# Performance work log

Measured on AMD Instinct MI355X. Metric: run time of the kernel, lower is better.

Reference implementation:

```python
import jax, jax.numpy as jnp
import numpy as np

UPDATE_RATE = 0.5
ALIVE_THRESH = 0.1

_SHIFTS = [(di, dj) for di in (-1, 0, 1) for dj in (-1, 0, 1) if not (di == 0 and dj == 0)]

def _laplacian(x):
    # circular 3x3 Laplacian: 8*center - 8 neighbors (wrap-around == circular pad)
    s = x * 8.0
    for di, dj in _SHIFTS:
        s = s - jnp.roll(x, (di, dj), axis=(2, 3))
    return s

def _alive_mask(alpha):
    # max_pool2d(3, stride=1) over circularly padded alpha == max over 3x3 wrap neighborhood
    m = alpha
    for di, dj in _SHIFTS:
        m = jnp.maximum(m, jnp.roll(alpha, (di, dj), axis=(2, 3)))
    return (m > ALIVE_THRESH).astype(alpha.dtype)

def setup_inputs() -> dict:
    key = jax.random.key(0)
    k1, k2, k3, k4, k5 = jax.random.split(key, 5)
    B, CHN, H, W = 4, 16, 512, 512
    PERC_N, HID = 2 * CHN, 192
    x = jax.random.uniform(k1, (B, CHN, H, W), dtype=jnp.float32)
    noise = jax.random.uniform(k2, (B, 1, H, W), dtype=jnp.float32)
    w1_w = jax.random.normal(k3, (HID, PERC_N), dtype=jnp.float32) * 0.1
    w1_b = jax.random.normal(k4, (HID,), dtype=jnp.float32) * 0.1
    w2_w = jax.random.normal(k5, (CHN, HID), dtype=jnp.float32) * 0.1
    return {"x": x, "noise": noise, "w1_w": w1_w, "w1_b": w1_b, "w2_w": w2_w}

def reference(x, noise, w1_w, w1_b, w2_w):
    alive = _alive_mask(x[:, 3:4])                       # [B,1,H,W]
    y = jnp.concatenate([x, _laplacian(x)], axis=1)      # [B,2C,H,W] perception
    h = jax.nn.relu(jnp.einsum('bchw,oc->bohw', y, w1_w) + w1_b[None, :, None, None])
    dx = jnp.einsum('bchw,oc->bohw', h, w2_w)            # [B,C,H,W]
    update_mask = jnp.floor(noise + UPDATE_RATE)         # stochastic per-pixel gate
    return (x + dx * update_mask) * alive
```

## Files before the change

### kernel.cpp

```cpp
#include <hip/hip_runtime.h>


#define HH 512
#define WW 512
#define CC 16
#define HID 192
#define NT 16
#define HW (HH * WW)

typedef _Float16 half8  __attribute__((ext_vector_type(8)));
typedef _Float16 half2v __attribute__((ext_vector_type(2)));
typedef __fp16   fp16x2 __attribute__((ext_vector_type(2)));
typedef float    f32x4  __attribute__((ext_vector_type(4)));
typedef unsigned int u32;

__device__ __forceinline__ u32 h2i(half2v v) { return __builtin_bit_cast(u32, v); }
__device__ __forceinline__ half2v i2h(u32 v) { return __builtin_bit_cast(half2v, v); }
__device__ __forceinline__ u32 pkrtz(float a, float b) {
    return __builtin_bit_cast(u32, __builtin_amdgcn_cvt_pkrtz(a, b));
}
__device__ __forceinline__ u32 fi(float f) { return __builtin_bit_cast(u32, f); }
__device__ __forceinline__ float if_(u32 v) { return __builtin_bit_cast(float, v); }

#define SWZ_P15 0x1F0
#define SWZ_P0  0x0010
#define SWZ_LO  0x000F

#define SWZ(v, patt) ((u32)__builtin_amdgcn_ds_swizzle((int)(v), (patt)))
#define DPP_UP1(old, src) ((u32)__builtin_amdgcn_update_dpp((int)(old), (int)(src), 0x111, 0xF, 0xF, false))
#define DPP_DN1(old, src) ((u32)__builtin_amdgcn_update_dpp((int)(old), (int)(src), 0x101, 0xF, 0xF, false))

__global__ __launch_bounds__(256, 2) void nca_mfma_kernel(
    const float* __restrict__ x,
    const float* __restrict__ noise,
    const float* __restrict__ w1w,
    const float* __restrict__ w1b,
    const float* __restrict__ w2w,
    float* __restrict__ out)
{
    __shared__ __align__(16) float bl[HID];
    const int tid  = threadIdx.x;
    const int lane = tid & 63;
    const int wid  = tid >> 6;
    const int p    = lane & 15;
    const int gq   = lane >> 4;

    const int bid = blockIdx.x;
    const int lin = (bid & 7) * 128 + (bid >> 3);
    const int gr    = __builtin_amdgcn_readfirstlane(lin * 4 + wid);
    const int b     = gr >> 10;
    const int rem   = gr & 1023;
    const int i     = rem >> 1;
    const int start = (rem & 1) * (WW / 2);

    for (int k = tid; k < HID; k += 256) bl[k] = w1b[k];
    __syncthreads();

    half8 w1f[12];
    #pragma unroll
    for (int t = 0; t < 12; ++t) {
        const float* src = w1w + (16 * t + p) * 32 + 8 * gq;
        #pragma unroll
        for (int e = 0; e < 8; ++e) w1f[t][e] = (_Float16)src[e];
    }
    const int pi_p = (p & 3) | ((p & 4) << 1) | ((p & 8) >> 1);
    half8 w2f[6];
    #pragma unroll
    for (int f = 0; f < 6; ++f) {
        const float* s0 = w2w + pi_p * HID + 32 * f + 4 * gq;
        #pragma unroll
        for (int e = 0; e < 4; ++e) {
            w2f[f][e]     = (_Float16)s0[e];
            w2f[f][4 + e] = (_Float16)s0[16 + e];
        }
    }

    const int im = (i == 0) ? HH - 1 : i - 1;
    const int ip = (i == HH - 1) ? 0 : i + 1;
    const int rT = im * WW, rM = i * WW, rB = ip * WW;
    const float* xbch = x + ((size_t)b * CC + 8 * (gq & 1)) * HW;
    const float* pT = xbch + rT;
    const float* pM = xbch + rM;
    const float* pB = xbch + rB;
    const float* nrow = noise + (size_t)b * HW + rM;
    float* orow = out + (size_t)b * CC * HW + rM;

    const bool hiSel = (gq >= 2);
    const int gqsw = ((gq & 1) << 1) | (gq >> 1);

    auto loadRaw = [&](int col, float r[24]) {
        #pragma unroll
        for (int e = 0; e < 8; ++e) {
            r[3 * e + 0] = pT[e * HW + col];
            r[3 * e + 1] = pM[e * HW + col];
            r[3 * e + 2] = pB[e * HW + col];
        }
    };
    auto combine = [&](const float r[24], half2v pcs[4], half2v pm[4],
                       float mx[4], float& cm) {
        #pragma unroll
        for (int w = 0; w < 4; ++w) {
            const float cs0 = r[6 * w + 0] + r[6 * w + 1] + r[6 * w + 2];
            const float cs1 = r[6 * w + 3] + r[6 * w + 4] + r[6 * w + 5];
            pcs[w] = i2h(pkrtz(cs0, cs1));
            pm[w]  = i2h(pkrtz(r[6 * w + 1], r[6 * w + 4]));
        }
        #pragma unroll
        for (int j = 0; j < 4; ++j)
            mx[j] = hiSel ? r[3 * (j + 4) + 1] : r[3 * j + 1];
        cm = fmaxf(fmaxf(r[9], r[10]), r[11]);
    };

    half2v pcsA[4], pcsB[4], pcsC[4], pmB[4], pmC[4];
    float  mxB[4], mxC[4];
    float  cmA, cmB, cmC;
    float  nzB, nzC;
    float  rr[24];

    {
        float rh[24]; half2v dum[4]; float dmx[4];
        loadRaw((start - 1) & (WW - 1), rh);
        combine(rh, pcsA, dum, dmx, cmA);
        float r0[24];
        loadRaw(start + p, r0);
        combine(r0, pcsB, pmB, mxB, cmB);
        float r1[24];
        loadRaw(start + 16 + p, r1);
        combine(r1, pcsC, pmC, mxC, cmC);
        nzB = nrow[start + p];
        nzC = nrow[start + 16 + p];
    }

    const f32x4* blv = (const f32x4*)bl;
    const half2v k9 = {(_Float16)9.0f, (_Float16)9.0f};
    const bool isCenter = (gq < 2);
    const u32 PZ = 0;

    #pragma unroll 4
    for (int t = 0; t < NT; ++t) {
        const int colP = (start + 16 * (t + 2) + p) & (WW - 1);
        loadRaw(colP, rr);
        const float nzD = nrow[colP];

        union { half8 v; u32 iw[4]; } yf;
        #pragma unroll
        for (int w = 0; w < 4; ++w) {
            const u32 bw = h2i(pcsB[w]);
            const u32 pl = SWZ(h2i(pcsA[w]), SWZ_P15);
            const u32 pr = SWZ(h2i(pcsC[w]), SWZ_P0);
            const u32 lft = DPP_UP1(pl, bw);
            const u32 rgt = DPP_DN1(pr, bw);
            const half2v s9  = i2h(lft) + i2h(bw) + i2h(rgt);
            const half2v lap = k9 * pmB[w] - s9;
            yf.iw[w] = isCenter ? h2i(pmB[w]) : h2i(lap);
        }

        const u32 pml = SWZ(fi(cmA), SWZ_P15);
        const u32 pmr = SWZ(fi(cmC), SWZ_P0);
        const float ml = if_(DPP_UP1(pml, fi(cmB)));
        const float mr = if_(DPP_DN1(pmr, fi(cmB)));
        const float rmax  = fmaxf(fmaxf(ml, cmB), mr);
        const float av    = if_(SWZ(fi(rmax), SWZ_LO));
        const float alive = (av > 0.1f) ? 1.0f : 0.0f;
        const float um    = floorf(nzB + 0.5f);

        f32x4 acc2a = {0.f, 0.f, 0.f, 0.f}, acc2b = {0.f, 0.f, 0.f, 0.f};
        #pragma unroll
        for (int f = 0; f < 6; ++f) {
            const f32x4 ba = blv[8 * f + gq];
            const f32x4 bb = blv[8 * f + 4 + gq];
            const f32x4 a1 = __builtin_amdgcn_mfma_f32_16x16x32_f16(w1f[2 * f],     yf.v, ba, 0, 0, 0);
            const f32x4 a2 = __builtin_amdgcn_mfma_f32_16x16x32_f16(w1f[2 * f + 1], yf.v, bb, 0, 0, 0);
            union { half8 v; u32 iw[4]; } hf;
            #pragma unroll
            for (int w = 0; w < 4; ++w) {
                const f32x4& aa = (w < 2) ? a1 : a2;
                const u32 pk = pkrtz(aa[2 * (w & 1)], aa[2 * (w & 1) + 1]);
                u32 rl;
                asm("v_pk_max_f16 %0, %1, %2" : "=v"(rl) : "v"(pk), "v"(PZ));
                hf.iw[w] = rl;
            }
            if (f & 1) acc2b = __builtin_amdgcn_mfma_f32_16x16x32_f16(w2f[f], hf.v, acc2b, 0, 0, 0);
            else       acc2a = __builtin_amdgcn_mfma_f32_16x16x32_f16(w2f[f], hf.v, acc2a, 0, 0, 0);
        }

        const int col = start + 16 * t + p;
        #pragma unroll
        for (int r = 0; r < 4; ++r) {
            const float dx = acc2a[r] + acc2b[r];
            orow[(size_t)(4 * gqsw + r) * HW + col] = (mxB[r] + dx * um) * alive;
        }

        half2v pcsD[4], pmD[4]; float mxD[4]; float cmD;
        combine(rr, pcsD, pmD, mxD, cmD);
        #pragma unroll
        for (int w = 0; w < 4; ++w) {
            pcsA[w] = pcsB[w];
            pcsB[w] = pcsC[w]; pmB[w] = pmC[w];
            pcsC[w] = pcsD[w]; pmC[w] = pmD[w];
        }
        #pragma unroll
        for (int j = 0; j < 4; ++j) { mxB[j] = mxC[j]; mxC[j] = mxD[j]; }
        cmA = cmB; cmB = cmC; cmC = cmD;
        nzB = nzC; nzC = nzD;
    }
}

extern "C" void kernel_launch(void* const* d_in, const int* in_sizes, int n_in,
                              void* d_out, int out_size, void* d_ws, size_t ws_size,
                              hipStream_t stream)
{
    const float* x     = (const float*)d_in[0];
    const float* noise = (const float*)d_in[1];
    const float* w1w   = (const float*)d_in[2];
    const float* w1b   = (const float*)d_in[3];
    const float* w2w   = (const float*)d_in[4];
    float* out = (float*)d_out;

    nca_mfma_kernel<<<1024, 256, 0, stream>>>(x, noise, w1w, w1b, w2w, out);
}
```

Measured before the change: 59.07 us.

## Fold Laplacian center term into W1, prefetch deeper, reuse fp16 center values

The 9*center part of the Laplacian is folded into the first-layer weights at load time, so the loop feeds the raw 3x3 neighbour sum into the MFMA instead of computing 9x−s9 per pixel. Column loads are moved one tile further ahead, so the fetch for column t+3 is in flight while column t is computed. The separate fp32 copy of the residual x is dropped, and the output residual is rebuilt from the packed fp16 center values. This cuts per-pixel ALU work and register pressure, but the residual now carries fp16 round-toward-zero error, and the deeper prefetch keeps more data live in registers.

```diff
diff --git a/kernel.cpp b/kernel.cpp
--- a/kernel.cpp
+++ b/kernel.cpp
@@ -10,7 +10,6 @@
 
 typedef _Float16 half8  __attribute__((ext_vector_type(8)));
 typedef _Float16 half2v __attribute__((ext_vector_type(2)));
-typedef __fp16   fp16x2 __attribute__((ext_vector_type(2)));
 typedef float    f32x4  __attribute__((ext_vector_type(4)));
 typedef unsigned int u32;
 
@@ -56,12 +55,18 @@
     for (int k = tid; k < HID; k += 256) bl[k] = w1b[k];
     __syncthreads();
 
+    const bool isCenter = (gq < 2);
     half8 w1f[12];
     #pragma unroll
     for (int t = 0; t < 12; ++t) {
-        const float* src = w1w + (16 * t + p) * 32 + 8 * gq;
-        #pragma unroll
-        for (int e = 0; e < 8; ++e) w1f[t][e] = (_Float16)src[e];
+        const float* src = w1w + (16 * t + p) * 32;
+        #pragma unroll
+        for (int e = 0; e < 8; ++e) {
+            const int o1 = 8 * gq + e;
+            const int o2 = o1 + (isCenter ? 16 : 0);
+            const float a = src[o1], c = src[o2];
+            w1f[t][e] = (_Float16)(isCenter ? (a + 9.0f * c) : -a);
+        }
     }
     const int pi_p = (p & 3) | ((p & 4) << 1) | ((p & 8) >> 1);
     half8 w2f[6];
@@ -96,8 +101,7 @@
             r[3 * e + 2] = pB[e * HW + col];
         }
     };
-    auto combine = [&](const float r[24], half2v pcs[4], half2v pm[4],
-                       float mx[4], float& cm) {
+    auto combine = [&](const float r[24], half2v pcs[4], half2v pm[4], float& cm) {
         #pragma unroll
         for (int w = 0; w < 4; ++w) {
             const float cs0 = r[6 * w + 0] + r[6 * w + 1] + r[6 * w + 2];
@@ -105,42 +109,41 @@
             pcs[w] = i2h(pkrtz(cs0, cs1));
             pm[w]  = i2h(pkrtz(r[6 * w + 1], r[6 * w + 4]));
         }
-        #pragma unroll
-        for (int j = 0; j < 4; ++j)
-            mx[j] = hiSel ? r[3 * (j + 4) + 1] : r[3 * j + 1];
         cm = fmaxf(fmaxf(r[9], r[10]), r[11]);
     };
 
     half2v pcsA[4], pcsB[4], pcsC[4], pmB[4], pmC[4];
-    float  mxB[4], mxC[4];
     float  cmA, cmB, cmC;
-    float  nzB, nzC;
+    float  nzB, nzC, nzD;
     float  rr[24];
 
     {
-        float rh[24]; half2v dum[4]; float dmx[4];
+        float rh[24]; half2v dum[4];
         loadRaw((start - 1) & (WW - 1), rh);
-        combine(rh, pcsA, dum, dmx, cmA);
+        combine(rh, pcsA, dum, cmA);
         float r0[24];
         loadRaw(start + p, r0);
-        combine(r0, pcsB, pmB, mxB, cmB);
+        combine(r0, pcsB, pmB, cmB);
         float r1[24];
         loadRaw(start + 16 + p, r1);
-        combine(r1, pcsC, pmC, mxC, cmC);
+        combine(r1, pcsC, pmC, cmC);
         nzB = nrow[start + p];
         nzC = nrow[start + 16 + p];
+        loadRaw(start + 32 + p, rr);
+        nzD = nrow[start + 32 + p];
     }
 
     const f32x4* blv = (const f32x4*)bl;
-    const half2v k9 = {(_Float16)9.0f, (_Float16)9.0f};
-    const bool isCenter = (gq < 2);
     const u32 PZ = 0;
 
     #pragma unroll 4
     for (int t = 0; t < NT; ++t) {
-        const int colP = (start + 16 * (t + 2) + p) & (WW - 1);
+        half2v pcsD[4], pmD[4]; float cmD;
+        combine(rr, pcsD, pmD, cmD);
+
+        const int colP = (start + 16 * (t + 3) + p) & (WW - 1);
         loadRaw(colP, rr);
-        const float nzD = nrow[colP];
+        const float nzE = nrow[colP];
 
         union { half8 v; u32 iw[4]; } yf;
         #pragma unroll
@@ -150,9 +153,8 @@
             const u32 pr = SWZ(h2i(pcsC[w]), SWZ_P0);
             const u32 lft = DPP_UP1(pl, bw);
             const u32 rgt = DPP_DN1(pr, bw);
-            const half2v s9  = i2h(lft) + i2h(bw) + i2h(rgt);
-            const half2v lap = k9 * pmB[w] - s9;
-            yf.iw[w] = isCenter ? h2i(pmB[w]) : h2i(lap);
+            const half2v s9 = i2h(lft) + i2h(bw) + i2h(rgt);
+            yf.iw[w] = isCenter ? h2i(pmB[w]) : h2i(s9);
         }
 
         const u32 pml = SWZ(fi(cmA), SWZ_P15);
@@ -184,25 +186,24 @@
             else       acc2a = __builtin_amdgcn_mfma_f32_16x16x32_f16(w2f[f], hf.v, acc2a, 0, 0, 0);
         }
 
+        const half2v xp0 = hiSel ? pmB[2] : pmB[0];
+        const half2v xp1 = hiSel ? pmB[3] : pmB[1];
+        const float xr[4] = {(float)xp0[0], (float)xp0[1], (float)xp1[0], (float)xp1[1]};
         const int col = start + 16 * t + p;
         #pragma unroll
         for (int r = 0; r < 4; ++r) {
             const float dx = acc2a[r] + acc2b[r];
-            orow[(size_t)(4 * gqsw + r) * HW + col] = (mxB[r] + dx * um) * alive;
-        }
-
-        half2v pcsD[4], pmD[4]; float mxD[4]; float cmD;
-        combine(rr, pcsD, pmD, mxD, cmD);
+            orow[(size_t)(4 * gqsw + r) * HW + col] = (xr[r] + dx * um) * alive;
+        }
+
         #pragma unroll
         for (int w = 0; w < 4; ++w) {
             pcsA[w] = pcsB[w];
             pcsB[w] = pcsC[w]; pmB[w] = pmC[w];
             pcsC[w] = pcsD[w]; pmC[w] = pmD[w];
         }
-        #pragma unroll
-        for (int j = 0; j < 4; ++j) { mxB[j] = mxC[j]; mxC[j] = mxD[j]; }
         cmA = cmB; cmB = cmC; cmC = cmD;
-        nzB = nzC; nzC = nzD;
+        nzB = nzC; nzC = nzD; nzD = nzE;
     }
 }
 
```

After: 73.41 us. 24.3% more time.

## Process two adjacent columns per lane with float2 loads and full-row waves

Applied to the files above, without the earlier changes.

Each lane now handles two adjacent pixels using 8-byte vector loads and stores instead of scalar accesses. Each wave processes a full image row, so the grid is halved to 512 blocks and the per-wave halo/prologue overhead is reduced. Horizontal neighbor exchange is restructured so that within-lane pairs avoid cross-lane shuffles and only the outer neighbors use swizzle/DPP. This doubles the MFMA work per iteration and raises register pressure, and the smaller grid (two blocks per CU via launch bounds) may leave parallelism or latency hiding insufficient.

```diff
diff --git a/kernel.cpp b/kernel.cpp
--- a/kernel.cpp
+++ b/kernel.cpp
@@ -10,7 +10,7 @@
 
 typedef _Float16 half8  __attribute__((ext_vector_type(8)));
 typedef _Float16 half2v __attribute__((ext_vector_type(2)));
-typedef __fp16   fp16x2 __attribute__((ext_vector_type(2)));
+typedef float    f32x2  __attribute__((ext_vector_type(2)));
 typedef float    f32x4  __attribute__((ext_vector_type(4)));
 typedef unsigned int u32;
 
@@ -25,7 +25,6 @@
 #define SWZ_P15 0x1F0
 #define SWZ_P0  0x0010
 #define SWZ_LO  0x000F
-
 #define SWZ(v, patt) ((u32)__builtin_amdgcn_ds_swizzle((int)(v), (patt)))
 #define DPP_UP1(old, src) ((u32)__builtin_amdgcn_update_dpp((int)(old), (int)(src), 0x111, 0xF, 0xF, false))
 #define DPP_DN1(old, src) ((u32)__builtin_amdgcn_update_dpp((int)(old), (int)(src), 0x101, 0xF, 0xF, false))
@@ -46,12 +45,10 @@
     const int gq   = lane >> 4;
 
     const int bid = blockIdx.x;
-    const int lin = (bid & 7) * 128 + (bid >> 3);
-    const int gr    = __builtin_amdgcn_readfirstlane(lin * 4 + wid);
-    const int b     = gr >> 10;
-    const int rem   = gr & 1023;
-    const int i     = rem >> 1;
-    const int start = (rem & 1) * (WW / 2);
+    const int lin = (bid & 7) * 64 + (bid >> 3);
+    const int gr  = __builtin_amdgcn_readfirstlane(lin * 4 + wid);
+    const int b   = gr >> 9;
+    const int i   = gr & 511;
 
     for (int k = tid; k < HID; k += 256) bl[k] = w1b[k];
     __syncthreads();
@@ -77,58 +74,72 @@
 
     const int im = (i == 0) ? HH - 1 : i - 1;
     const int ip = (i == HH - 1) ? 0 : i + 1;
-    const int rT = im * WW, rM = i * WW, rB = ip * WW;
     const float* xbch = x + ((size_t)b * CC + 8 * (gq & 1)) * HW;
-    const float* pT = xbch + rT;
-    const float* pM = xbch + rM;
-    const float* pB = xbch + rB;
-    const float* nrow = noise + (size_t)b * HW + rM;
-    float* orow = out + (size_t)b * CC * HW + rM;
+    const float* pT = xbch + im * WW;
+    const float* pM = xbch + (size_t)i * WW;
+    const float* pB = xbch + ip * WW;
+    const float* nrow = noise + (size_t)b * HW + (size_t)i * WW;
+    float* orow = out + (size_t)b * CC * HW + (size_t)i * WW;
 
     const bool hiSel = (gq >= 2);
     const int gqsw = ((gq & 1) << 1) | (gq >> 1);
 
-    auto loadRaw = [&](int col, float r[24]) {
+    f32x2 rT[8], rM[8], rB[8];
+    auto loadRaw2 = [&](int base) {
+        const int col = base + 2 * p;
         #pragma unroll
         for (int e = 0; e < 8; ++e) {
-            r[3 * e + 0] = pT[e * HW + col];
-            r[3 * e + 1] = pM[e * HW + col];
-            r[3 * e + 2] = pB[e * HW + col];
+            rT[e] = *(const f32x2*)(pT + e * HW + col);
+            rM[e] = *(const f32x2*)(pM + e * HW + col);
+            rB[e] = *(const f32x2*)(pB + e * HW + col);
         }
     };
-    auto combine = [&](const float r[24], half2v pcs[4], half2v pm[4],
-                       float mx[4], float& cm) {
+    auto combine2 = [&](u32 csw[2][4], u32 pmw[2][4], float mx[2][4], float cm[2]) {
+        #pragma unroll
+        for (int s = 0; s < 2; ++s) {
+            #pragma unroll
+            for (int w = 0; w < 4; ++w) {
+                const float c0 = rT[2 * w][s] + rM[2 * w][s] + rB[2 * w][s];
+                const float c1 = rT[2 * w + 1][s] + rM[2 * w + 1][s] + rB[2 * w + 1][s];
+                csw[s][w] = pkrtz(c0, c1);
+                pmw[s][w] = pkrtz(rM[2 * w][s], rM[2 * w + 1][s]);
+            }
+            #pragma unroll
+            for (int j = 0; j < 4; ++j)
+                mx[s][j] = hiSel ? rM[j + 4][s] : rM[j][s];
+            cm[s] = fmaxf(fmaxf(rT[3][s], rM[3][s]), rB[3][s]);
+        }
+    };
+
+    u32  cswB[2][4], pmwB[2][4], cswC[2][4], pmwC[2][4];
+    float mxB[2][4], mxC[2][4];
+    float cmB[2], cmC[2];
+    f32x2 nzB, nzC;
+    u32  cswA1[4];
+    float cmA1;
+
+    {
+        float ht[8], hm[8], hb[8];
+        #pragma unroll
+        for (int e = 0; e < 8; ++e) {
+            ht[e] = pT[e * HW + (WW - 1)];
+            hm[e] = pM[e * HW + (WW - 1)];
+            hb[e] = pB[e * HW + (WW - 1)];
+        }
         #pragma unroll
         for (int w = 0; w < 4; ++w) {
-            const float cs0 = r[6 * w + 0] + r[6 * w + 1] + r[6 * w + 2];
-            const float cs1 = r[6 * w + 3] + r[6 * w + 4] + r[6 * w + 5];
-            pcs[w] = i2h(pkrtz(cs0, cs1));
-            pm[w]  = i2h(pkrtz(r[6 * w + 1], r[6 * w + 4]));
-        }
-        #pragma unroll
-        for (int j = 0; j < 4; ++j)
-            mx[j] = hiSel ? r[3 * (j + 4) + 1] : r[3 * j + 1];
-        cm = fmaxf(fmaxf(r[9], r[10]), r[11]);
-    };
-
-    half2v pcsA[4], pcsB[4], pcsC[4], pmB[4], pmC[4];
-    float  mxB[4], mxC[4];
-    float  cmA, cmB, cmC;
-    float  nzB, nzC;
-    float  rr[24];
-
-    {
-        float rh[24]; half2v dum[4]; float dmx[4];
-        loadRaw((start - 1) & (WW - 1), rh);
-        combine(rh, pcsA, dum, dmx, cmA);
-        float r0[24];
-        loadRaw(start + p, r0);
-        combine(r0, pcsB, pmB, mxB, cmB);
-        float r1[24];
-        loadRaw(start + 16 + p, r1);
-        combine(r1, pcsC, pmC, mxC, cmC);
-        nzB = nrow[start + p];
-        nzC = nrow[start + 16 + p];
+            const float c0 = ht[2 * w] + hm[2 * w] + hb[2 * w];
+            const float c1 = ht[2 * w + 1] + hm[2 * w + 1] + hb[2 * w + 1];
+            cswA1[w] = pkrtz(c0, c1);
+        }
+        cmA1 = fmaxf(fmaxf(ht[3], hm[3]), hb[3]);
+
+        loadRaw2(0);
+        combine2(cswB, pmwB, mxB, cmB);
+        nzB = *(const f32x2*)(nrow + 2 * p);
+        loadRaw2(32);
+        combine2(cswC, pmwC, mxC, cmC);
+        nzC = *(const f32x2*)(nrow + 32 + 2 * p);
     }
 
     const f32x4* blv = (const f32x4*)bl;
@@ -136,41 +147,14 @@
     const bool isCenter = (gq < 2);
     const u32 PZ = 0;
 
-    #pragma unroll 4
-    for (int t = 0; t < NT; ++t) {
-        const int colP = (start + 16 * (t + 2) + p) & (WW - 1);
-        loadRaw(colP, rr);
-        const float nzD = nrow[colP];
-
-        union { half8 v; u32 iw[4]; } yf;
-        #pragma unroll
-        for (int w = 0; w < 4; ++w) {
-            const u32 bw = h2i(pcsB[w]);
-            const u32 pl = SWZ(h2i(pcsA[w]), SWZ_P15);
-            const u32 pr = SWZ(h2i(pcsC[w]), SWZ_P0);
-            const u32 lft = DPP_UP1(pl, bw);
-            const u32 rgt = DPP_DN1(pr, bw);
-            const half2v s9  = i2h(lft) + i2h(bw) + i2h(rgt);
-            const half2v lap = k9 * pmB[w] - s9;
-            yf.iw[w] = isCenter ? h2i(pmB[w]) : h2i(lap);
-        }
-
-        const u32 pml = SWZ(fi(cmA), SWZ_P15);
-        const u32 pmr = SWZ(fi(cmC), SWZ_P0);
-        const float ml = if_(DPP_UP1(pml, fi(cmB)));
-        const float mr = if_(DPP_DN1(pmr, fi(cmB)));
-        const float rmax  = fmaxf(fmaxf(ml, cmB), mr);
-        const float av    = if_(SWZ(fi(rmax), SWZ_LO));
-        const float alive = (av > 0.1f) ? 1.0f : 0.0f;
-        const float um    = floorf(nzB + 0.5f);
-
+    auto gemm = [&](const half8& yv, float dx[4]) {
         f32x4 acc2a = {0.f, 0.f, 0.f, 0.f}, acc2b = {0.f, 0.f, 0.f, 0.f};
         #pragma unroll
         for (int f = 0; f < 6; ++f) {
             const f32x4 ba = blv[8 * f + gq];
             const f32x4 bb = blv[8 * f + 4 + gq];
-            const f32x4 a1 = __builtin_amdgcn_mfma_f32_16x16x32_f16(w1f[2 * f],     yf.v, ba, 0, 0, 0);
-            const f32x4 a2 = __builtin_amdgcn_mfma_f32_16x16x32_f16(w1f[2 * f + 1], yf.v, bb, 0, 0, 0);
+            const f32x4 a1 = __builtin_amdgcn_mfma_f32_16x16x32_f16(w1f[2 * f],     yv, ba, 0, 0, 0);
+            const f32x4 a2 = __builtin_amdgcn_mfma_f32_16x16x32_f16(w1f[2 * f + 1], yv, bb, 0, 0, 0);
             union { half8 v; u32 iw[4]; } hf;
             #pragma unroll
             for (int w = 0; w < 4; ++w) {
@@ -183,25 +167,70 @@
             if (f & 1) acc2b = __builtin_amdgcn_mfma_f32_16x16x32_f16(w2f[f], hf.v, acc2b, 0, 0, 0);
             else       acc2a = __builtin_amdgcn_mfma_f32_16x16x32_f16(w2f[f], hf.v, acc2a, 0, 0, 0);
         }
-
-        const int col = start + 16 * t + p;
+        #pragma unroll
+        for (int r = 0; r < 4; ++r) dx[r] = acc2a[r] + acc2b[r];
+    };
+
+    #pragma unroll 4
+    for (int T = 0; T < NT; ++T) {
+        const int baseP = (32 * (T + 2)) & (WW - 1);
+        loadRaw2(baseP);
+        const f32x2 nzD = *(const f32x2*)(nrow + baseP + 2 * p);
+
+        union { half8 v; u32 iw[4]; } yf0, yf1;
+        #pragma unroll
+        for (int w = 0; w < 4; ++w) {
+            const u32 lft0 = DPP_UP1(SWZ(cswA1[w], SWZ_P15), cswB[1][w]);
+            const half2v s90 = i2h(lft0) + i2h(cswB[0][w]) + i2h(cswB[1][w]);
+            const half2v lap0 = k9 * i2h(pmwB[0][w]) - s90;
+            yf0.iw[w] = isCenter ? pmwB[0][w] : h2i(lap0);
+            const u32 rgt1 = DPP_DN1(SWZ(cswC[0][w], SWZ_P0), cswB[0][w]);
+            const half2v s91 = i2h(cswB[0][w]) + i2h(cswB[1][w]) + i2h(rgt1);
+            const half2v lap1 = k9 * i2h(pmwB[1][w]) - s91;
+            yf1.iw[w] = isCenter ? pmwB[1][w] : h2i(lap1);
+        }
+
+        const float ml0 = if_(DPP_UP1(SWZ(fi(cmA1), SWZ_P15), fi(cmB[1])));
+        const float rmax0 = fmaxf(fmaxf(ml0, cmB[0]), cmB[1]);
+        const float alive0 = (if_(SWZ(fi(rmax0), SWZ_LO)) > 0.1f) ? 1.0f : 0.0f;
+        const float mr1 = if_(DPP_DN1(SWZ(fi(cmC[0]), SWZ_P0), fi(cmB[0])));
+        const float rmax1 = fmaxf(fmaxf(cmB[0], cmB[1]), mr1);
+        const float alive1 = (if_(SWZ(fi(rmax1), SWZ_LO)) > 0.1f) ? 1.0f : 0.0f;
+        const float um0 = floorf(nzB[0] + 0.5f);
+        const float um1 = floorf(nzB[1] + 0.5f);
+
+        float dx0[4], dx1[4];
+        gemm(yf0.v, dx0);
+        gemm(yf1.v, dx1);
+
+        const int col = 32 * T + 2 * p;
         #pragma unroll
         for (int r = 0; r < 4; ++r) {
-            const float dx = acc2a[r] + acc2b[r];
-            orow[(size_t)(4 * gqsw + r) * HW + col] = (mxB[r] + dx * um) * alive;
-        }
-
-        half2v pcsD[4], pmD[4]; float mxD[4]; float cmD;
-        combine(rr, pcsD, pmD, mxD, cmD);
+            f32x2 v;
+            v[0] = (mxB[0][r] + dx0[r] * um0) * alive0;
+            v[1] = (mxB[1][r] + dx1[r] * um1) * alive1;
+            *(f32x2*)(orow + (size_t)(4 * gqsw + r) * HW + col) = v;
+        }
+
+        u32 cswD[2][4], pmwD[2][4]; float mxD[2][4]; float cmD[2];
+        combine2(cswD, pmwD, mxD, cmD);
+        #pragma unroll
+        for (int w = 0; w < 4; ++w) cswA1[w] = cswB[1][w];
+        cmA1 = cmB[1];
         #pragma unroll
         for (int w = 0; w < 4; ++w) {
-            pcsA[w] = pcsB[w];
-            pcsB[w] = pcsC[w]; pmB[w] = pmC[w];
-            pcsC[w] = pcsD[w]; pmC[w] = pmD[w];
-        }
-        #pragma unroll
-        for (int j = 0; j < 4; ++j) { mxB[j] = mxC[j]; mxC[j] = mxD[j]; }
-        cmA = cmB; cmB = cmC; cmC = cmD;
+            #pragma unroll
+            for (int s = 0; s < 2; ++s) {
+                cswB[s][w] = cswC[s][w]; pmwB[s][w] = pmwC[s][w];
+                cswC[s][w] = cswD[s][w]; pmwC[s][w] = pmwD[s][w];
+            }
+        }
+        #pragma unroll
+        for (int s = 0; s < 2; ++s) {
+            #pragma unroll
+            for (int j = 0; j < 4; ++j) { mxB[s][j] = mxC[s][j]; mxC[s][j] = mxD[s][j]; }
+            cmB[s] = cmC[s]; cmC[s] = cmD[s];
+        }
         nzB = nzC; nzC = nzD;
     }
 }
@@ -217,5 +246,5 @@
     const float* w2w   = (const float*)d_in[4];
     float* out = (float*)d_out;
 
-    nca_mfma_kernel<<<1024, 256, 0, stream>>>(x, noise, w1w, w1b, w2w, out);
+    nca_mfma_kernel<<<512, 256, 0, stream>>>(x, noise, w1w, w1b, w2w, out);
 }
```

New measurement: 215.2 us. 264% more time.
